# Optimization experiments

Measured on AMD Instinct MI355X. Metric: run time of the kernel, lower is better.

Reference implementation:

```python
import jax, jax.numpy as jnp
import numpy as np

N, D, H, E = 16384, 1024, 4096, 8

def setup_inputs() -> dict:
    key = jax.random.key(0)
    ks = jax.random.split(key, 7)
    s = 0.02
    return {
        "x": jax.random.normal(ks[0], (N, D), dtype=jnp.float32),
        "Ws": jax.random.normal(ks[1], (H, D), dtype=jnp.float32) * s,
        "bs": jax.random.normal(ks[2], (H,), dtype=jnp.float32) * s,
        "We": jax.random.normal(ks[3], (E, H, D), dtype=jnp.float32) * s,
        "be": jax.random.normal(ks[4], (E, H), dtype=jnp.float32) * s,
        "Wr": jax.random.normal(ks[5], (E, D), dtype=jnp.float32) * s,
        "br": jax.random.normal(ks[6], (E,), dtype=jnp.float32) * s,
    }

def reference(x, Ws, bs, We, be, Wr, br):
    # shared FFN: [N, H]
    shared = x @ Ws.T + bs
    # router: softmax over experts, top-1 via argmax (argmax(softmax)==argmax(logits), kept faithful)
    expert_scores = jax.nn.softmax(x @ Wr.T + br, axis=-1)  # [N, E]
    token_expert = jnp.argmax(expert_scores, axis=-1)       # [N]
    # mask-accumulate over the small fixed expert set (dense per-expert FFN as in source)
    routed = jnp.zeros_like(shared)
    num_experts = We.shape[0]
    for i in range(num_experts):
        mask = (token_expert == i).astype(shared.dtype)[:, None]  # [N, 1]
        routed = routed + mask * (x @ We[i].T + be[i])
    return shared + routed
```

## Files before the change

### kernel.cpp

```cpp
#include <hip/hip_runtime.h>
#include <stdint.h>

#define N_TOK 16384
#define DDIM  1024
#define HDIM  4096
#define NEXP  8
#define BM    256
#define MAXMT 72
#define MAXNR 5

typedef __attribute__((ext_vector_type(8))) short short8;
typedef __attribute__((ext_vector_type(4))) float f32x4;

__device__ __forceinline__ unsigned short f2b(float f) {
    union { float f; unsigned int u; } x; x.f = f;
    unsigned int r = x.u + 0x7FFFu + ((x.u >> 16) & 1u);
    return (unsigned short)(r >> 16);
}

__global__ __launch_bounds__(256)
void k_router_cast(const float* __restrict__ x, const float* __restrict__ Wr,
                   const float* __restrict__ br, unsigned short* __restrict__ xb,
                   int* __restrict__ eid)
{
    __shared__ float wr[NEXP * DDIM];
    const int t = threadIdx.x;
    for (int i = t; i < NEXP * DDIM / 4; i += 256)
        ((float4*)wr)[i] = ((const float4*)Wr)[i];
    __syncthreads();
    const int lane = t & 63;
    const int n = blockIdx.x * 4 + (t >> 6);
    const float* xr = x + (size_t)n * DDIM;
    double acc[NEXP];
#pragma unroll
    for (int e = 0; e < NEXP; ++e) acc[e] = 0.0;
#pragma unroll
    for (int j = 0; j < 4; ++j) {
        const int d = j * 256 + lane * 4;
        float4 v = *(const float4*)(xr + d);
        unsigned long long pk =
            (unsigned long long)(f2b(v.x) | ((unsigned int)f2b(v.y) << 16)) |
            ((unsigned long long)(f2b(v.z) | ((unsigned int)f2b(v.w) << 16)) << 32);
        *(unsigned long long*)(xb + (size_t)n * DDIM + d) = pk;
#pragma unroll
        for (int e = 0; e < NEXP; ++e) {
            const float* w = wr + e * DDIM + d;
            acc[e] += (double)v.x * (double)w[0];
            acc[e] += (double)v.y * (double)w[1];
            acc[e] += (double)v.z * (double)w[2];
            acc[e] += (double)v.w * (double)w[3];
        }
    }
#pragma unroll
    for (int e = 0; e < NEXP; ++e)
#pragma unroll
        for (int off = 32; off > 0; off >>= 1)
            acc[e] += __shfl_down(acc[e], off);
    if (lane == 0) {
        double best = acc[0] + (double)br[0];
        int bi = 0;
#pragma unroll
        for (int e = 1; e < NEXP; ++e) {
            double v = acc[e] + (double)br[e];
            if (v > best) { best = v; bi = e; }
        }
        eid[n] = bi;
    }
}

__global__ __launch_bounds__(256)
void k_hist(const int* __restrict__ eid, int* __restrict__ counts)
{
    __shared__ int h[NEXP];
    const int t = threadIdx.x;
    if (t < NEXP) h[t] = 0;
    __syncthreads();
    atomicAdd(&h[eid[blockIdx.x * 256 + t]], 1);
    __syncthreads();
    if (t < NEXP && h[t]) atomicAdd(&counts[t * 16], h[t]);
}

__global__ void k_scan(const int* __restrict__ counts, int* __restrict__ texp,
                       int* __restrict__ pbase)
{
    if (threadIdx.x == 0) {
        int tt = 0;
        for (int e = 0; e < NEXP; ++e) {
            pbase[e] = tt * BM;
            const int nt = (counts[e * 16] + BM - 1) / BM;
            for (int i = 0; i < nt; ++i) texp[tt++] = e;
        }
        pbase[8] = tt;
        for (; tt < MAXMT; ++tt) texp[tt] = -1;
    }
}

__global__ __launch_bounds__(256)
void k_scatter(const int* __restrict__ eid, const int* __restrict__ pbase,
               int* __restrict__ cursors, int* __restrict__ perm)
{
    __shared__ int h[NEXP];
    __shared__ int base[NEXP];
    const int t = threadIdx.x;
    if (t < NEXP) h[t] = 0;
    __syncthreads();
    const int n = blockIdx.x * 256 + t;
    const int e = eid[n];
    const int rank = atomicAdd(&h[e], 1);
    __syncthreads();
    if (t < NEXP) base[t] = h[t] ? atomicAdd(&cursors[t * 16], h[t]) : 0;
    __syncthreads();
    perm[pbase[e] + base[e] + rank] = n;
}

__global__ __launch_bounds__(256)
void k_combine_w(const float* __restrict__ Ws, const float* __restrict__ We,
                 unsigned short* __restrict__ wc)
{
    const size_t i = ((size_t)blockIdx.x * 256 + threadIdx.x) * 8;
    const size_t hd = i & (size_t)(HDIM * DDIM - 1);
    float4 a0 = *(const float4*)(We + i);
    float4 a1 = *(const float4*)(We + i + 4);
    float4 b0 = *(const float4*)(Ws + hd);
    float4 b1 = *(const float4*)(Ws + hd + 4);
    uint4 o;
    o.x = f2b(a0.x + b0.x) | ((unsigned)f2b(a0.y + b0.y) << 16);
    o.y = f2b(a0.z + b0.z) | ((unsigned)f2b(a0.w + b0.w) << 16);
    o.z = f2b(a1.x + b1.x) | ((unsigned)f2b(a1.y + b1.y) << 16);
    o.w = f2b(a1.z + b1.z) | ((unsigned)f2b(a1.w + b1.w) << 16);
    *(uint4*)(wc + i) = o;
}

__global__ __launch_bounds__(256)
void k_combine_b(const float* __restrict__ bs, const float* __restrict__ be,
                 float* __restrict__ bc)
{
    const int i = blockIdx.x * 256 + threadIdx.x;
    bc[i] = bs[i & (HDIM - 1)] + be[i];
}

#define SBAR()   __builtin_amdgcn_s_barrier()
#define SCHED0() __builtin_amdgcn_sched_barrier(0)
#define LGKM0()  asm volatile("s_waitcnt lgkmcnt(0)" ::: "memory")

__global__ __launch_bounds__(512, 2)
void k_gemm(const unsigned short* __restrict__ X, const unsigned short* __restrict__ W,
            const float* __restrict__ bc, const int* __restrict__ perm,
            const int* __restrict__ texp, const int* __restrict__ realM_p,
            float* __restrict__ out)
{
    __shared__ unsigned short lds[65536];
    __shared__ int   toksLDS[MAXNR][256];
    __shared__ float biasLDS[MAXNR][256];

    const int realM = realM_p[8];
    const int base  = blockIdx.x;
    const int tnr   = base & 15;
    const int tmB   = base >> 4;
    const int nR    = (realM - tmB + 15) >> 4;
    const int T     = nR << 4;

    const int t    = threadIdx.x;
    const int lane = t & 63;
    const int wid  = t >> 6;
    const int wm   = wid >> 2;
    const int wn   = wid & 3;

    const int srow    = t >> 3;
    const int schunkE = (((t & 7) ^ (srow & 7)) << 3);
    unsigned short* dstT = lds + (t << 3);

    const int rA   = lane & 15;
    const int c0   = ((lane >> 4) << 3) ^ ((lane & 7) << 3);
    const int c1   = c0 ^ 32;
    const int aBase = ((2 + wm) << 13) + (rA << 6);
    const int bBase = ((wn >> 1) << 13) + ((wn & 1) << 12) + (rA << 6);
    const int colBase = tnr * 256 + wn * 64 + rA;

    int ePk = 0;
#pragma unroll
    for (int w = 0; w < MAXNR; ++w) {
        const int ev = (w < nR) ? texp[tmB + (w << 4)] : 0;
        ePk |= (ev & 15) << (w << 2);
    }
    if (t < 256) {
#pragma unroll
        for (int w = 0; w < MAXNR; ++w) {
            if (w < nR) {
                toksLDS[w][t] = perm[(tmB + (w << 4)) * 256 + t];
                const int ev = (ePk >> (w << 2)) & 15;
                biasLDS[w][t] = bc[ev * HDIM + tnr * 256 + t];
            }
        }
    }
    __syncthreads();

    int tokCur[4], tokNext[4];
#pragma unroll
    for (int i = 0; i < 4; ++i) {
        int a = toksLDS[0][i * 64 + srow];
        tokCur[i] = a < 0 ? 0 : a;
        int b = (nR > 1) ? toksLDS[1][i * 64 + srow] : 0;
        tokNext[i] = b < 0 ? 0 : b;
    }

    f32x4 acc[8][4];
    {
        float bn[4];
#pragma unroll
        for (int n = 0; n < 4; ++n) bn[n] = biasLDS[0][wn * 64 + n * 16 + rA];
#pragma unroll
        for (int m = 0; m < 8; ++m)
#pragma unroll
            for (int n = 0; n < 4; ++n)
                acc[m][n] = (f32x4){bn[n], bn[n], bn[n], bn[n]};
    }
    short8 fa[8][2], fb[4][2];

    auto STAGE = [&](int sg, int tau) {
        if (sg >= (nR << 6)) return;
        const int tloc = sg >> 2;
        const int h    = sg & 3;
        const int kb   = (tloc & 15) << 6;
        unsigned short* d = dstT + ((tloc & 1) << 15) + (h << 13);
        const unsigned short *s0, *s1;
        if (h < 2) {
            const int wS = tloc >> 4;
            const int ee = (ePk >> (wS << 2)) & 15;
            const size_t r0 = (size_t)(ee * HDIM + tnr * 256 + h * 128 + srow) * DDIM
                              + schunkE + kb;
            s0 = W + r0; s1 = W + r0 + (size_t)64 * DDIM;
        } else {
            const bool nxt = (tloc >> 4) != (tau >> 4);
            const int i0 = (h - 2) << 1;
            const int ta = nxt ? tokNext[i0]     : tokCur[i0];
            const int tb = nxt ? tokNext[i0 + 1] : tokCur[i0 + 1];
            s0 = X + (size_t)ta * DDIM + schunkE + kb;
            s1 = X + (size_t)tb * DDIM + schunkE + kb;
        }
        __builtin_amdgcn_global_load_lds(
            (const __attribute__((address_space(1))) void*)s0,
            (__attribute__((address_space(3))) void*)d, 16, 0, 0);
        __builtin_amdgcn_global_load_lds(
            (const __attribute__((address_space(1))) void*)s1,
            (__attribute__((address_space(3))) void*)(d + 4096), 16, 0, 0);
    };

#define LDA(m) \
    fa[m][0] = *(const short8*)&lds[bufOff + aBase + (m)*1024 + c0]; \
    fa[m][1] = *(const short8*)&lds[bufOff + aBase + (m)*1024 + c1];
#define LDB(n) \
    fb[n][0] = *(const short8*)&lds[bufOff + bBase + (n)*1024 + c0]; \
    fb[n][1] = *(const short8*)&lds[bufOff + bBase + (n)*1024 + c1];
#define MM(m,n) \
    acc[m][n] = __builtin_amdgcn_mfma_f32_16x16x32_bf16(fa[m][0], fb[n][0], acc[m][n], 0,0,0); \
    acc[m][n] = __builtin_amdgcn_mfma_f32_16x16x32_bf16(fa[m][1], fb[n][1], acc[m][n], 0,0,0);

#pragma unroll
    for (int s = 0; s < 7; ++s) STAGE(s, 0);
    asm volatile("s_waitcnt vmcnt(6)" ::: "memory");
    SCHED0(); SBAR(); SCHED0();

    int w = 0;
#pragma unroll 1
    for (int tau = 0; tau < T; ++tau) {
        const int tt = tau & 15;
        const int bufOff = (tau & 1) << 15;
        const int sig = (tau << 2) + 7;

        LDB(0) LDB(1) LDB(2) LDB(3) LDA(0) LDA(1)
        SCHED0();
        LDA(2) LDA(3)
        SCHED0();
        LDA(4) LDA(5) LDA(6) LDA(7)
        STAGE(sig, tau);
        SCHED0();
        asm volatile("s_waitcnt lgkmcnt(12)" ::: "memory"); SCHED0();
        __builtin_amdgcn_s_setprio(1);
        MM(0,0) MM(0,1) MM(0,2) MM(0,3) MM(1,0) MM(1,1) MM(1,2) MM(1,3)
        __builtin_amdgcn_s_setprio(0); SCHED0();
        asm volatile("s_waitcnt lgkmcnt(8)" ::: "memory"); SCHED0();
        __builtin_amdgcn_s_setprio(1);
        MM(2,0) MM(2,1) MM(2,2) MM(2,3) MM(3,0) MM(3,1) MM(3,2) MM(3,3)
        __builtin_amdgcn_s_setprio(0); SCHED0();
        LGKM0(); SBAR(); SCHED0();
        STAGE(sig + 1, tau); STAGE(sig + 2, tau); STAGE(sig + 3, tau);
        SCHED0();
        __builtin_amdgcn_s_setprio(1);
        MM(4,0) MM(4,1) MM(4,2) MM(4,3) MM(5,0) MM(5,1) MM(5,2) MM(5,3)
        MM(6,0) MM(6,1) MM(6,2) MM(6,3) MM(7,0) MM(7,1) MM(7,2) MM(7,3)
        __builtin_amdgcn_s_setprio(0); SCHED0();
        if (tau < T - 2)       { asm volatile("s_waitcnt vmcnt(6)" ::: "memory"); }
        else if (tau == T - 2) { asm volatile("s_waitcnt vmcnt(0)" ::: "memory"); }
        SBAR(); SCHED0();

        if (tt == 15) {
            const int rsub = (lane >> 4) * 4;
#pragma unroll
            for (int m = 0; m < 8; ++m) {
                const int rl = wm * 128 + m * 16 + rsub;
                int tk[4];
#pragma unroll
                for (int j = 0; j < 4; ++j) tk[j] = toksLDS[w][rl + j];
#pragma unroll
                for (int n = 0; n < 4; ++n) {
                    const int col = colBase + n * 16;
#pragma unroll
                    for (int j = 0; j < 4; ++j)
                        if (tk[j] >= 0) out[(size_t)tk[j] * HDIM + col] = acc[m][n][j];
                }
            }
            if (w + 1 < nR) {
                float bn[4];
#pragma unroll
                for (int n = 0; n < 4; ++n) bn[n] = biasLDS[w + 1][wn * 64 + n * 16 + rA];
#pragma unroll
                for (int m = 0; m < 8; ++m)
#pragma unroll
                    for (int n = 0; n < 4; ++n)
                        acc[m][n] = (f32x4){bn[n], bn[n], bn[n], bn[n]};
#pragma unroll
                for (int i = 0; i < 4; ++i) tokCur[i] = tokNext[i];
                if (w + 2 < nR) {
#pragma unroll
                    for (int i = 0; i < 4; ++i) {
                        int v = toksLDS[w + 2][i * 64 + srow];
                        tokNext[i] = v < 0 ? 0 : v;
                    }
                }
            }
            ++w;
        }
    }
#undef LDA
#undef LDB
#undef MM
}

extern "C" void kernel_launch(void* const* d_in, const int* in_sizes, int n_in,
                              void* d_out, int out_size, void* d_ws, size_t ws_size,
                              hipStream_t stream)
{
    const float* x  = (const float*)d_in[0];
    const float* Ws = (const float*)d_in[1];
    const float* bs = (const float*)d_in[2];
    const float* We = (const float*)d_in[3];
    const float* be = (const float*)d_in[4];
    const float* Wr = (const float*)d_in[5];
    const float* br = (const float*)d_in[6];
    float* out = (float*)d_out;
    char* ws = (char*)d_ws;

    unsigned short* xb  = (unsigned short*)(ws + 0);
    unsigned short* wc  = (unsigned short*)(ws + 33554432);
    float*          bc  = (float*)(ws + 100663296);
    int*            eid = (int*)(ws + 100794368);
    int*            perm= (int*)(ws + 100859904);
    int*            cnt = (int*)(ws + 100933632);
    int*            cur = (int*)(ws + 100934144);
    int*            pb  = (int*)(ws + 100934656);
    int*            texp= (int*)(ws + 100934720);

    hipMemsetAsync(perm, 0xFF, MAXMT * BM * sizeof(int), stream);
    hipMemsetAsync(cnt, 0, 1024, stream);

    k_router_cast<<<N_TOK / 4, 256, 0, stream>>>(x, Wr, br, xb, eid);
    k_combine_w<<<(NEXP * (size_t)HDIM * DDIM / 8) / 256, 256, 0, stream>>>(Ws, We, wc);
    k_combine_b<<<NEXP * HDIM / 256, 256, 0, stream>>>(bs, be, bc);
    k_hist<<<N_TOK / 256, 256, 0, stream>>>(eid, cnt);
    k_scan<<<1, 64, 0, stream>>>(cnt, texp, pb);
    k_scatter<<<N_TOK / 256, 256, 0, stream>>>(eid, pb, cur, perm);
    k_gemm<<<256, 512, 0, stream>>>(xb, wc, bc, perm, texp, pb, out);
}
```

Baseline: 283.3 us.

## Restructure GEMM into 4-slot K=32 pipeline with one barrier per step

The K step shrinks from 64 to 32 and the single-buffered-per-parity LDS layout becomes a 4-slot ring. Each thread now loads one token row and one weight row per stage, with loads issued three stages ahead. One of the two barriers per iteration and the swizzled layout are removed, which cuts synchronisation and gives loads more time to arrive. The trade-off is twice as many loop iterations, and the unswizzled LDS layout may cause bank conflicts.

Measured after the change: 378.9 us. +33.7%, slower.

```diff
diff --git a/kernel.cpp b/kernel.cpp
--- a/kernel.cpp
+++ b/kernel.cpp
@@ -141,7 +141,6 @@
 
 #define SBAR()   __builtin_amdgcn_s_barrier()
 #define SCHED0() __builtin_amdgcn_sched_barrier(0)
-#define LGKM0()  asm volatile("s_waitcnt lgkmcnt(0)" ::: "memory")
 
 __global__ __launch_bounds__(512, 2)
 void k_gemm(const unsigned short* __restrict__ X, const unsigned short* __restrict__ W,
@@ -158,7 +157,7 @@
     const int tnr   = base & 15;
     const int tmB   = base >> 4;
     const int nR    = (realM - tmB + 15) >> 4;
-    const int T     = nR << 4;
+    const int T     = nR << 5;
 
     const int t    = threadIdx.x;
     const int lane = t & 63;
@@ -166,16 +165,14 @@
     const int wm   = wid >> 2;
     const int wn   = wid & 3;
 
-    const int srow    = t >> 3;
-    const int schunkE = (((t & 7) ^ (srow & 7)) << 3);
+    const int rA   = lane & 15;
+    const int rBase = ((lane >> 4) << 12) + (rA << 4);
+    const int aOffW = (wm << 11);
+    const int colBase = tnr * 256 + wn * 64 + rA;
+
+    const int srcRow = t & 255;
+    const int kcHi   = t >> 8;
     unsigned short* dstT = lds + (t << 3);
-
-    const int rA   = lane & 15;
-    const int c0   = ((lane >> 4) << 3) ^ ((lane & 7) << 3);
-    const int c1   = c0 ^ 32;
-    const int aBase = ((2 + wm) << 13) + (rA << 6);
-    const int bBase = ((wn >> 1) << 13) + ((wn & 1) << 12) + (rA << 6);
-    const int colBase = tnr * 256 + wn * 64 + rA;
 
     int ePk = 0;
 #pragma unroll
@@ -195,13 +192,10 @@
     }
     __syncthreads();
 
-    int tokCur[4], tokNext[4];
-#pragma unroll
-    for (int i = 0; i < 4; ++i) {
-        int a = toksLDS[0][i * 64 + srow];
-        tokCur[i] = a < 0 ? 0 : a;
-        int b = (nR > 1) ? toksLDS[1][i * 64 + srow] : 0;
-        tokNext[i] = b < 0 ? 0 : b;
+    int tokC, tokN;
+    {
+        int a = toksLDS[0][srcRow];  tokC = a < 0 ? 0 : a;
+        int b = (nR > 1) ? toksLDS[1][srcRow] : 0;  tokN = b < 0 ? 0 : b;
     }
 
     f32x4 acc[8][4];
@@ -215,86 +209,74 @@
             for (int n = 0; n < 4; ++n)
                 acc[m][n] = (f32x4){bn[n], bn[n], bn[n], bn[n]};
     }
-    short8 fa[8][2], fb[4][2];
-
-    auto STAGE = [&](int sg, int tau) {
-        if (sg >= (nR << 6)) return;
-        const int tloc = sg >> 2;
-        const int h    = sg & 3;
-        const int kb   = (tloc & 15) << 6;
-        unsigned short* d = dstT + ((tloc & 1) << 15) + (h << 13);
-        const unsigned short *s0, *s1;
-        if (h < 2) {
-            const int wS = tloc >> 4;
-            const int ee = (ePk >> (wS << 2)) & 15;
-            const size_t r0 = (size_t)(ee * HDIM + tnr * 256 + h * 128 + srow) * DDIM
-                              + schunkE + kb;
-            s0 = W + r0; s1 = W + r0 + (size_t)64 * DDIM;
-        } else {
-            const bool nxt = (tloc >> 4) != (tau >> 4);
-            const int i0 = (h - 2) << 1;
-            const int ta = nxt ? tokNext[i0]     : tokCur[i0];
-            const int tb = nxt ? tokNext[i0 + 1] : tokCur[i0 + 1];
-            s0 = X + (size_t)ta * DDIM + schunkE + kb;
-            s1 = X + (size_t)tb * DDIM + schunkE + kb;
-        }
+    short8 fa[8], fb[4];
+
+    auto STAGE = [&](int st, int tau) {
+        if (st >= T) return;
+        const int kb   = (st & 31) << 5;
+        const int stW  = st >> 5;
+        unsigned short* d = dstT + ((st & 3) << 14);
+        const int tok = (stW == (tau >> 5)) ? tokC : tokN;
+        const unsigned short* sA = X + (size_t)tok * DDIM + kb + (kcHi << 3);
+        const int ee = (ePk >> (stW << 2)) & 15;
+        const unsigned short* sB =
+            W + ((size_t)ee * HDIM + (size_t)tnr * 256 + srcRow) * DDIM + kb + (kcHi << 3);
         __builtin_amdgcn_global_load_lds(
-            (const __attribute__((address_space(1))) void*)s0,
+            (const __attribute__((address_space(1))) void*)sA,
             (__attribute__((address_space(3))) void*)d, 16, 0, 0);
         __builtin_amdgcn_global_load_lds(
-            (const __attribute__((address_space(1))) void*)s1,
+            (const __attribute__((address_space(1))) void*)(sA + 16),
             (__attribute__((address_space(3))) void*)(d + 4096), 16, 0, 0);
+        __builtin_amdgcn_global_load_lds(
+            (const __attribute__((address_space(1))) void*)sB,
+            (__attribute__((address_space(3))) void*)(d + 8192), 16, 0, 0);
+        __builtin_amdgcn_global_load_lds(
+            (const __attribute__((address_space(1))) void*)(sB + 16),
+            (__attribute__((address_space(3))) void*)(d + 12288), 16, 0, 0);
     };
 
-#define LDA(m) \
-    fa[m][0] = *(const short8*)&lds[bufOff + aBase + (m)*1024 + c0]; \
-    fa[m][1] = *(const short8*)&lds[bufOff + aBase + (m)*1024 + c1];
-#define LDB(n) \
-    fb[n][0] = *(const short8*)&lds[bufOff + bBase + (n)*1024 + c0]; \
-    fb[n][1] = *(const short8*)&lds[bufOff + bBase + (n)*1024 + c1];
-#define MM(m,n) \
-    acc[m][n] = __builtin_amdgcn_mfma_f32_16x16x32_bf16(fa[m][0], fb[n][0], acc[m][n], 0,0,0); \
-    acc[m][n] = __builtin_amdgcn_mfma_f32_16x16x32_bf16(fa[m][1], fb[n][1], acc[m][n], 0,0,0);
-
-#pragma unroll
-    for (int s = 0; s < 7; ++s) STAGE(s, 0);
-    asm volatile("s_waitcnt vmcnt(6)" ::: "memory");
+#define LDA(m) fa[m] = *(const short8*)((const char*)lds + slotB + rBase + aOffW + ((m) << 8));
+#define LDB(n) fb[n] = *(const short8*)((const char*)lds + slotB + 16384 + rBase + (wn << 10) + ((n) << 8));
+#define MM(m,n) acc[m][n] = __builtin_amdgcn_mfma_f32_16x16x32_bf16(fa[m], fb[n], acc[m][n], 0,0,0);
+
+    STAGE(0, 0); STAGE(1, 0); STAGE(2, 0);
+    asm volatile("s_waitcnt vmcnt(8)" ::: "memory");
     SCHED0(); SBAR(); SCHED0();
 
     int w = 0;
 #pragma unroll 1
     for (int tau = 0; tau < T; ++tau) {
-        const int tt = tau & 15;
-        const int bufOff = (tau & 1) << 15;
-        const int sig = (tau << 2) + 7;
-
+        const int tt = tau & 31;
+        const int slotB = (tau & 3) << 15;
+
+        STAGE(tau + 3, tau);
+        SCHED0();
         LDB(0) LDB(1) LDB(2) LDB(3) LDA(0) LDA(1)
         SCHED0();
-        LDA(2) LDA(3)
+        LDA(2) LDA(3) LDA(4)
         SCHED0();
-        LDA(4) LDA(5) LDA(6) LDA(7)
-        STAGE(sig, tau);
+        LDA(5) LDA(6) LDA(7)
         SCHED0();
-        asm volatile("s_waitcnt lgkmcnt(12)" ::: "memory"); SCHED0();
+        asm volatile("s_waitcnt lgkmcnt(6)" ::: "memory"); SCHED0();
         __builtin_amdgcn_s_setprio(1);
         MM(0,0) MM(0,1) MM(0,2) MM(0,3) MM(1,0) MM(1,1) MM(1,2) MM(1,3)
         __builtin_amdgcn_s_setprio(0); SCHED0();
-        asm volatile("s_waitcnt lgkmcnt(8)" ::: "memory"); SCHED0();
+        asm volatile("s_waitcnt lgkmcnt(3)" ::: "memory"); SCHED0();
         __builtin_amdgcn_s_setprio(1);
         MM(2,0) MM(2,1) MM(2,2) MM(2,3) MM(3,0) MM(3,1) MM(3,2) MM(3,3)
+        MM(4,0) MM(4,1) MM(4,2) MM(4,3)
         __builtin_amdgcn_s_setprio(0); SCHED0();
-        LGKM0(); SBAR(); SCHED0();
-        STAGE(sig + 1, tau); STAGE(sig + 2, tau); STAGE(sig + 3, tau);
-        SCHED0();
+        asm volatile("s_waitcnt lgkmcnt(0)" ::: "memory"); SCHED0();
         __builtin_amdgcn_s_setprio(1);
-        MM(4,0) MM(4,1) MM(4,2) MM(4,3) MM(5,0) MM(5,1) MM(5,2) MM(5,3)
-        MM(6,0) MM(6,1) MM(6,2) MM(6,3) MM(7,0) MM(7,1) MM(7,2) MM(7,3)
+        MM(5,0) MM(5,1) MM(5,2) MM(5,3) MM(6,0) MM(6,1) MM(6,2) MM(6,3)
+        MM(7,0) MM(7,1) MM(7,2) MM(7,3)
         __builtin_amdgcn_s_setprio(0); SCHED0();
-        if (tau < T - 2)       { asm volatile("s_waitcnt vmcnt(6)" ::: "memory"); }
+        if (tau < T - 3)       { asm volatile("s_waitcnt vmcnt(8)" ::: "memory"); }
+        else if (tau == T - 3) { asm volatile("s_waitcnt vmcnt(4)" ::: "memory"); }
         else if (tau == T - 2) { asm volatile("s_waitcnt vmcnt(0)" ::: "memory"); }
         SBAR(); SCHED0();
 
-        if (tt == 15) {
+        if (tt == 31) {
             const int rsub = (lane >> 4) * 4;
 #pragma unroll
             for (int m = 0; m < 8; ++m) {
@@ -319,14 +301,10 @@
 #pragma unroll
                     for (int n = 0; n < 4; ++n)
                         acc[m][n] = (f32x4){bn[n], bn[n], bn[n], bn[n]};
-#pragma unroll
-                for (int i = 0; i < 4; ++i) tokCur[i] = tokNext[i];
+                tokC = tokN;
                 if (w + 2 < nR) {
-#pragma unroll
-                    for (int i = 0; i < 4; ++i) {
-                        int v = toksLDS[w + 2][i * 64 + srow];
-                        tokNext[i] = v < 0 ? 0 : v;
-                    }
+                    int v = toksLDS[w + 2][srcRow];
+                    tokN = v < 0 ? 0 : v;
                 }
             }
             ++w;
```

## Fuse router, weight-combine and bias kernels; fold scan into scatter and GEMM

Applied to the files above, without the earlier changes.

Merges the router/cast, weight-combine and bias-combine kernels into one launch that dispatches on block index range. Removes the single-thread scan kernel by having the scatter kernel and the GEMM recompute per-expert tile prefix sums from the counts directly. This cuts several kernel launches and their serialization gaps. The fused kernel's static shared memory allocation applies to every block, which may reduce occupancy for the memory-bound weight-combine blocks.

Result: faster. 271.2 us, median of 2 (-4.3%).

```diff
diff --git a/kernel.cpp b/kernel.cpp
--- a/kernel.cpp
+++ b/kernel.cpp
@@ -9,6 +9,10 @@
 #define MAXMT 72
 #define MAXNR 5
 
+#define GRID_R 4096
+#define GRID_W 16384
+#define GRID_B 128
+
 typedef __attribute__((ext_vector_type(8))) short short8;
 typedef __attribute__((ext_vector_type(4))) float f32x4;
 
@@ -19,52 +23,76 @@
 }
 
 __global__ __launch_bounds__(256)
-void k_router_cast(const float* __restrict__ x, const float* __restrict__ Wr,
-                   const float* __restrict__ br, unsigned short* __restrict__ xb,
-                   int* __restrict__ eid)
-{
-    __shared__ float wr[NEXP * DDIM];
+void k_fused(const float* __restrict__ x, const float* __restrict__ Wr,
+             const float* __restrict__ br, unsigned short* __restrict__ xb,
+             int* __restrict__ eid,
+             const float* __restrict__ Ws, const float* __restrict__ We,
+             unsigned short* __restrict__ wc,
+             const float* __restrict__ bs, const float* __restrict__ be,
+             float* __restrict__ bc)
+{
+    const int bid = blockIdx.x;
     const int t = threadIdx.x;
-    for (int i = t; i < NEXP * DDIM / 4; i += 256)
-        ((float4*)wr)[i] = ((const float4*)Wr)[i];
-    __syncthreads();
-    const int lane = t & 63;
-    const int n = blockIdx.x * 4 + (t >> 6);
-    const float* xr = x + (size_t)n * DDIM;
-    double acc[NEXP];
-#pragma unroll
-    for (int e = 0; e < NEXP; ++e) acc[e] = 0.0;
-#pragma unroll
-    for (int j = 0; j < 4; ++j) {
-        const int d = j * 256 + lane * 4;
-        float4 v = *(const float4*)(xr + d);
-        unsigned long long pk =
-            (unsigned long long)(f2b(v.x) | ((unsigned int)f2b(v.y) << 16)) |
-            ((unsigned long long)(f2b(v.z) | ((unsigned int)f2b(v.w) << 16)) << 32);
-        *(unsigned long long*)(xb + (size_t)n * DDIM + d) = pk;
-#pragma unroll
-        for (int e = 0; e < NEXP; ++e) {
-            const float* w = wr + e * DDIM + d;
-            acc[e] += (double)v.x * (double)w[0];
-            acc[e] += (double)v.y * (double)w[1];
-            acc[e] += (double)v.z * (double)w[2];
-            acc[e] += (double)v.w * (double)w[3];
-        }
-    }
-#pragma unroll
-    for (int e = 0; e < NEXP; ++e)
-#pragma unroll
-        for (int off = 32; off > 0; off >>= 1)
-            acc[e] += __shfl_down(acc[e], off);
-    if (lane == 0) {
-        double best = acc[0] + (double)br[0];
-        int bi = 0;
-#pragma unroll
-        for (int e = 1; e < NEXP; ++e) {
-            double v = acc[e] + (double)br[e];
-            if (v > best) { best = v; bi = e; }
-        }
-        eid[n] = bi;
+
+    if (bid < GRID_R) {
+        __shared__ float wr[NEXP * DDIM];
+        for (int i = t; i < NEXP * DDIM / 4; i += 256)
+            ((float4*)wr)[i] = ((const float4*)Wr)[i];
+        __syncthreads();
+        const int lane = t & 63;
+        const int n = bid * 4 + (t >> 6);
+        const float* xr = x + (size_t)n * DDIM;
+        double acc[NEXP];
+#pragma unroll
+        for (int e = 0; e < NEXP; ++e) acc[e] = 0.0;
+#pragma unroll
+        for (int j = 0; j < 4; ++j) {
+            const int d = j * 256 + lane * 4;
+            float4 v = *(const float4*)(xr + d);
+            unsigned long long pk =
+                (unsigned long long)(f2b(v.x) | ((unsigned int)f2b(v.y) << 16)) |
+                ((unsigned long long)(f2b(v.z) | ((unsigned int)f2b(v.w) << 16)) << 32);
+            *(unsigned long long*)(xb + (size_t)n * DDIM + d) = pk;
+#pragma unroll
+            for (int e = 0; e < NEXP; ++e) {
+                const float* w = wr + e * DDIM + d;
+                acc[e] += (double)v.x * (double)w[0];
+                acc[e] += (double)v.y * (double)w[1];
+                acc[e] += (double)v.z * (double)w[2];
+                acc[e] += (double)v.w * (double)w[3];
+            }
+        }
+#pragma unroll
+        for (int e = 0; e < NEXP; ++e)
+#pragma unroll
+            for (int off = 32; off > 0; off >>= 1)
+                acc[e] += __shfl_down(acc[e], off);
+        if (lane == 0) {
+            double best = acc[0] + (double)br[0];
+            int bi = 0;
+#pragma unroll
+            for (int e = 1; e < NEXP; ++e) {
+                double v = acc[e] + (double)br[e];
+                if (v > best) { best = v; bi = e; }
+            }
+            eid[n] = bi;
+        }
+    } else if (bid < GRID_R + GRID_W) {
+        const size_t i = ((size_t)(bid - GRID_R) * 256 + t) * 8;
+        const size_t hd = i & (size_t)(HDIM * DDIM - 1);
+        float4 a0 = *(const float4*)(We + i);
+        float4 a1 = *(const float4*)(We + i + 4);
+        float4 b0 = *(const float4*)(Ws + hd);
+        float4 b1 = *(const float4*)(Ws + hd + 4);
+        uint4 o;
+        o.x = f2b(a0.x + b0.x) | ((unsigned)f2b(a0.y + b0.y) << 16);
+        o.y = f2b(a0.z + b0.z) | ((unsigned)f2b(a0.w + b0.w) << 16);
+        o.z = f2b(a1.x + b1.x) | ((unsigned)f2b(a1.y + b1.y) << 16);
+        o.w = f2b(a1.z + b1.z) | ((unsigned)f2b(a1.w + b1.w) << 16);
+        *(uint4*)(wc + i) = o;
+    } else {
+        const int i = (bid - GRID_R - GRID_W) * 256 + t;
+        bc[i] = bs[i & (HDIM - 1)] + be[i];
     }
 }
 
@@ -80,63 +108,28 @@
     if (t < NEXP && h[t]) atomicAdd(&counts[t * 16], h[t]);
 }
 
-__global__ void k_scan(const int* __restrict__ counts, int* __restrict__ texp,
-                       int* __restrict__ pbase)
-{
-    if (threadIdx.x == 0) {
-        int tt = 0;
-        for (int e = 0; e < NEXP; ++e) {
-            pbase[e] = tt * BM;
-            const int nt = (counts[e * 16] + BM - 1) / BM;
-            for (int i = 0; i < nt; ++i) texp[tt++] = e;
-        }
-        pbase[8] = tt;
-        for (; tt < MAXMT; ++tt) texp[tt] = -1;
-    }
-}
-
 __global__ __launch_bounds__(256)
-void k_scatter(const int* __restrict__ eid, const int* __restrict__ pbase,
+void k_scatter(const int* __restrict__ eid, const int* __restrict__ counts,
                int* __restrict__ cursors, int* __restrict__ perm)
 {
+    __shared__ int cl[NEXP];
     __shared__ int h[NEXP];
     __shared__ int base[NEXP];
     const int t = threadIdx.x;
-    if (t < NEXP) h[t] = 0;
+    if (t < NEXP) { cl[t] = counts[t * 16]; h[t] = 0; }
     __syncthreads();
     const int n = blockIdx.x * 256 + t;
     const int e = eid[n];
+    int p = 0;
+#pragma unroll
+    for (int ee = 0; ee < NEXP; ++ee)
+        if (ee < e) p += (cl[ee] + 255) >> 8;
+    const int pbase = p << 8;
     const int rank = atomicAdd(&h[e], 1);
     __syncthreads();
     if (t < NEXP) base[t] = h[t] ? atomicAdd(&cursors[t * 16], h[t]) : 0;
     __syncthreads();
-    perm[pbase[e] + base[e] + rank] = n;
-}
-
-__global__ __launch_bounds__(256)
-void k_combine_w(const float* __restrict__ Ws, const float* __restrict__ We,
-                 unsigned short* __restrict__ wc)
-{
-    const size_t i = ((size_t)blockIdx.x * 256 + threadIdx.x) * 8;
-    const size_t hd = i & (size_t)(HDIM * DDIM - 1);
-    float4 a0 = *(const float4*)(We + i);
-    float4 a1 = *(const float4*)(We + i + 4);
-    float4 b0 = *(const float4*)(Ws + hd);
-    float4 b1 = *(const float4*)(Ws + hd + 4);
-    uint4 o;
-    o.x = f2b(a0.x + b0.x) | ((unsigned)f2b(a0.y + b0.y) << 16);
-    o.y = f2b(a0.z + b0.z) | ((unsigned)f2b(a0.w + b0.w) << 16);
-    o.z = f2b(a1.x + b1.x) | ((unsigned)f2b(a1.y + b1.y) << 16);
-    o.w = f2b(a1.z + b1.z) | ((unsigned)f2b(a1.w + b1.w) << 16);
-    *(uint4*)(wc + i) = o;
-}
-
-__global__ __launch_bounds__(256)
-void k_combine_b(const float* __restrict__ bs, const float* __restrict__ be,
-                 float* __restrict__ bc)
-{
-    const int i = blockIdx.x * 256 + threadIdx.x;
-    bc[i] = bs[i & (HDIM - 1)] + be[i];
+    perm[pbase + base[e] + rank] = n;
 }
 
 #define SBAR()   __builtin_amdgcn_s_barrier()
@@ -146,19 +139,24 @@
 __global__ __launch_bounds__(512, 2)
 void k_gemm(const unsigned short* __restrict__ X, const unsigned short* __restrict__ W,
             const float* __restrict__ bc, const int* __restrict__ perm,
-            const int* __restrict__ texp, const int* __restrict__ realM_p,
-            float* __restrict__ out)
+            const int* __restrict__ cnt, float* __restrict__ out)
 {
     __shared__ unsigned short lds[65536];
     __shared__ int   toksLDS[MAXNR][256];
     __shared__ float biasLDS[MAXNR][256];
 
-    const int realM = realM_p[8];
     const int base  = blockIdx.x;
     const int tnr   = base & 15;
     const int tmB   = base >> 4;
-    const int nR    = (realM - tmB + 15) >> 4;
-    const int T     = nR << 4;
+
+    int ntE[NEXP]; int realM = 0;
+#pragma unroll
+    for (int e = 0; e < NEXP; ++e) {
+        ntE[e] = (cnt[e * 16] + 255) >> 8;
+        realM += ntE[e];
+    }
+    const int nR = (realM - tmB + 15) >> 4;
+    const int T  = nR << 4;
 
     const int t    = threadIdx.x;
     const int lane = t & 63;
@@ -180,7 +178,16 @@
     int ePk = 0;
 #pragma unroll
     for (int w = 0; w < MAXNR; ++w) {
-        const int ev = (w < nR) ? texp[tmB + (w << 4)] : 0;
+        int ev = 0;
+        if (w < nR) {
+            const int tmW = tmB + (w << 4);
+            int pre = 0;
+#pragma unroll
+            for (int e = 0; e < NEXP; ++e) {
+                if (tmW >= pre) ev = e;
+                pre += ntE[e];
+            }
+        }
         ePk |= (ev & 15) << (w << 2);
     }
     if (t < 256) {
@@ -358,17 +365,13 @@
     int*            perm= (int*)(ws + 100859904);
     int*            cnt = (int*)(ws + 100933632);
     int*            cur = (int*)(ws + 100934144);
-    int*            pb  = (int*)(ws + 100934656);
-    int*            texp= (int*)(ws + 100934720);
 
     hipMemsetAsync(perm, 0xFF, MAXMT * BM * sizeof(int), stream);
     hipMemsetAsync(cnt, 0, 1024, stream);
 
-    k_router_cast<<<N_TOK / 4, 256, 0, stream>>>(x, Wr, br, xb, eid);
-    k_combine_w<<<(NEXP * (size_t)HDIM * DDIM / 8) / 256, 256, 0, stream>>>(Ws, We, wc);
-    k_combine_b<<<NEXP * HDIM / 256, 256, 0, stream>>>(bs, be, bc);
+    k_fused<<<GRID_R + GRID_W + GRID_B, 256, 0, stream>>>(
+        x, Wr, br, xb, eid, Ws, We, wc, bs, be, bc);
     k_hist<<<N_TOK / 256, 256, 0, stream>>>(eid, cnt);
-    k_scan<<<1, 64, 0, stream>>>(cnt, texp, pb);
-    k_scatter<<<N_TOK / 256, 256, 0, stream>>>(eid, pb, cur, perm);
-    k_gemm<<<256, 512, 0, stream>>>(xb, wc, bc, perm, texp, pb, out);
-}
+    k_scatter<<<N_TOK / 256, 256, 0, stream>>>(eid, cnt, cur, perm);
+    k_gemm<<<256, 512, 0, stream>>>(xb, wc, bc, perm, cnt, out);
+}
```
